# Optimization experiments

Measured on AMD Instinct MI355X. Metric: run time of the kernel, lower is better.

The kernel has to match this reference:

```python
import jax, jax.numpy as jnp
import numpy as np

N = 10000      # nodes
E = 320000     # edges (before self loops)
IN = 256
HID = 64
H = 8
OUT = 64
NEG_SLOPE = 0.2


def setup_inputs() -> dict:
    key = jax.random.key(0)
    ks = jax.random.split(key, 12)
    def glorot(k, shape):
        fan = sum(shape) if len(shape) == 2 else int(np.prod(shape))
        return jax.random.normal(k, shape, jnp.float32) * np.sqrt(2.0 / fan)
    x = jax.random.normal(ks[0], (N, IN), jnp.float32)
    edge_index = jax.random.randint(ks[1], (2, E), 0, N, jnp.int32)
    # positive weights so log2 is finite
    edge_weight = jax.random.uniform(ks[2], (E,), jnp.float32, 0.1, 1.0)
    return {
        'x': x, 'edge_index': edge_index, 'edge_weight': edge_weight,
        'W1': glorot(ks[3], (IN, H * HID)),
        'as1': glorot(ks[4], (H, HID)), 'ad1': glorot(ks[5], (H, HID)),
        'b1': jnp.zeros((H * HID,), jnp.float32),
        'W2': glorot(ks[6], (H * HID, H * OUT)),
        'as2': glorot(ks[7], (H, OUT)), 'ad2': glorot(ks[8], (H, OUT)),
        'b2': jnp.zeros((H * OUT,), jnp.float32),
    }


def _gat_conv(x, src, dst, log2_ew, W, att_src, att_dst, bias, heads, ch):
    n = x.shape[0]
    h = (x @ W).reshape(n, heads, ch)                      # [N,H,C]
    al_src = jnp.einsum('nhc,hc->nh', h, att_src)          # [N,H]
    al_dst = jnp.einsum('nhc,hc->nh', h, att_dst)
    alpha = al_src[src] + al_dst[dst]                      # [E,H]
    alpha = jax.nn.leaky_relu(alpha, NEG_SLOPE)
    alpha = alpha + log2_ew[:, None]
    # segment softmax over destination nodes (self loops ensure nonempty segments)
    amax = jax.ops.segment_max(alpha, dst, num_segments=n)
    ex = jnp.exp(alpha - amax[dst])
    denom = jax.ops.segment_sum(ex, dst, num_segments=n)
    alpha = ex / denom[dst]                                # [E,H]
    msg = h[src] * alpha[:, :, None]                       # [E,H,C]
    out = jax.ops.segment_sum(msg, dst, num_segments=n)    # [N,H,C]
    return out.reshape(n, heads * ch) + bias


def reference(x, edge_index, edge_weight, W1, as1, ad1, b1, W2, as2, ad2, b2):
    n = x.shape[0]
    # add self loops with fill_value = 1.0 (log2(1) = 0)
    loops = jnp.arange(n, dtype=edge_index.dtype)
    src = jnp.concatenate([edge_index[0], loops])
    dst = jnp.concatenate([edge_index[1], loops])
    ew = jnp.concatenate([edge_weight, jnp.ones((n,), edge_weight.dtype)])
    log2_ew = jnp.log2(ew)
    h = _gat_conv(x, src, dst, log2_ew, W1, as1, ad1, b1, H, HID)
    h = jax.nn.relu(h)  # dropout skipped (eval mode)
    out = _gat_conv(h, src, dst, log2_ew, W2, as2, ad2, b2, H, OUT)
    return out
```

## Files before the change

### kernel.cpp

```cpp
#include <hip/hip_runtime.h>
#include <hip/hip_bf16.h>

#define NN 10000
#define EE 320000
#define ETOT (EE + NN)
#define CIN 256
#define HC 512
#define NHEAD 8
#define NEG 0.2f

#define SX (NN * CIN)
#define SATT (6 * 512)

using bf16x8 = __attribute__((ext_vector_type(8))) short;
using f32x4 = __attribute__((ext_vector_type(4))) float;
typedef unsigned short u16;
typedef unsigned int u32;

__device__ __forceinline__ u16 f2bf(float f) {
  __hip_bfloat16 b = __float2bfloat16(f);
  return *(u16*)&b;
}
__device__ __forceinline__ float bflo(u32 p) { return __uint_as_float(p << 16); }
__device__ __forceinline__ float bfhi(u32 p) { return __uint_as_float(p & 0xFFFF0000u); }

#define PB_X ((SX + 255) / 256)
#define PB_ATT ((SATT + 255) / 256)
#define PB_CNT ((ETOT + 255) / 256)
#define PB_WT 96
#define PB_TOT (PB_X + PB_ATT + PB_CNT + PB_WT)

__global__ __launch_bounds__(256) void prep_k(
    const void* __restrict__ x, const void* __restrict__ w1,
    const void* __restrict__ w2,
    const void* a0, const void* a1, const void* a2,
    const void* a3, const void* a4, const void* a5,
    const int* __restrict__ ei,
    u16* __restrict__ xb, u16* __restrict__ w1t, u16* __restrict__ w2t,
    float* __restrict__ attf, int* __restrict__ counts, int* __restrict__ flag) {
  const int b = blockIdx.x, t = threadIdx.x;
  __shared__ int sbad;
  if (t == 0) sbad = 0;
  __syncthreads();
  {
    const u16* xu = (const u16*)x;
    unsigned e0 = (xu[2 * t] >> 7) & 0xFFu;
    unsigned e1 = (xu[2 * t + 1] >> 7) & 0xFFu;
    if (e0 >= 0xC8u || e1 >= 0xC8u) sbad = 1;
  }
  __syncthreads();
  const bool bf = (sbad == 0);
  if (b == 0 && t == 0) *flag = bf ? 1 : 0;

  if (b < PB_X) {
    if (!bf) {
      int i = b * 256 + t;
      if (i < SX) xb[i] = f2bf(((const float*)x)[i]);
    }
  } else if (b < PB_X + PB_ATT) {
    int j = (b - PB_X) * 256 + t;
    if (j < SATT) {
      const void* ps[6] = {a0, a1, a2, a3, a4, a5};
      const void* p = ps[j >> 9];
      int k = j & 511;
      attf[j] = bf ? __bfloat162float(((const __hip_bfloat16*)p)[k])
                   : ((const float*)p)[k];
    }
  } else if (b < PB_X + PB_ATT + PB_CNT) {
    int e = (b - PB_X - PB_ATT) * 256 + t;
    if (e < ETOT) {
      int d = (e < EE) ? ei[EE + e] : (e - EE);
      atomicAdd(&counts[d], 1);
    }
  } else {
    __shared__ u16 tile[64][72];
    int wb = b - (PB_X + PB_ATT + PB_CNT);
    const void* src;
    u16* dst;
    int K, tk, tn;
    if (wb < 32) { src = w1; dst = w1t; K = CIN; tk = (wb >> 3) * 64; tn = (wb & 7) * 64; }
    else { wb -= 32; src = w2; dst = w2t; K = HC; tk = (wb >> 3) * 64; tn = (wb & 7) * 64; }
    const int r = t >> 2, cb = (t & 3) * 16;
    if (bf) {
      const u16* s = (const u16*)src + (size_t)(tk + r) * HC + tn + cb;
      *(int4*)&tile[r][cb] = ((const int4*)s)[0];
      *(int4*)&tile[r][cb + 8] = ((const int4*)s)[1];
    } else {
      const float* s = (const float*)src + (size_t)(tk + r) * HC + tn + cb;
#pragma unroll
      for (int j = 0; j < 16; j++) tile[r][cb + j] = f2bf(s[j]);
    }
    __syncthreads();
    union { u16 o[16]; int4 v[2]; } u;
#pragma unroll
    for (int j = 0; j < 16; j++) u.o[j] = tile[cb + j][r];
    int4* dp = (int4*)(dst + (size_t)(tn + r) * K + tk + cb);
    dp[0] = u.v[0];
    dp[1] = u.v[1];
  }
}

__global__ __launch_bounds__(1024) void scan_k(const int* __restrict__ counts,
                                               int* __restrict__ rowptr,
                                               int* __restrict__ wcur) {
  __shared__ int buf[1024];
  const int t = threadIdx.x;
  int loc[10];
  int s = 0;
#pragma unroll
  for (int j = 0; j < 10; j++) {
    int i = t * 10 + j;
    s += (i < NN) ? counts[i] : 0;
    loc[j] = s;
  }
  buf[t] = s;
  __syncthreads();
  for (int off = 1; off < 1024; off <<= 1) {
    int v = (t >= off) ? buf[t - off] : 0;
    __syncthreads();
    buf[t] += v;
    __syncthreads();
  }
  int base = (t > 0) ? buf[t - 1] : 0;
  int prev = 0;
#pragma unroll
  for (int j = 0; j < 10; j++) {
    int i = t * 10 + j;
    if (i < NN) {
      rowptr[i + 1] = base + loc[j];
      wcur[i] = base + prev;
    }
    prev = loc[j];
  }
  if (t == 0) rowptr[0] = 0;
}

__global__ void fill_k(const int* __restrict__ ei, const void* __restrict__ ew,
                       const int* __restrict__ flag, int* __restrict__ wcur,
                       int* __restrict__ esrc, float* __restrict__ elw) {
  int e = blockIdx.x * blockDim.x + threadIdx.x;
  if (e >= ETOT) return;
  int s, d;
  float lw;
  if (e < EE) {
    s = ei[e];
    d = ei[EE + e];
    float w = (*flag) ? __bfloat162float(((const __hip_bfloat16*)ew)[e])
                      : ((const float*)ew)[e];
    lw = log2f(w);
  } else {
    s = d = e - EE;
    lw = 0.f;
  }
  int pos = atomicAdd(&wcur[d], 1);
  esrc[pos] = s;
  elw[pos] = lw;
}

#define BM 64
#define BN 128
#define BK 64
#define LSTR 72

__global__ __launch_bounds__(256) void gemm_mfma(const u16* __restrict__ A,
                                                 const void* __restrict__ Axalt,
                                                 const int* __restrict__ flagp,
                                                 const u16* __restrict__ Wt,
                                                 const float* __restrict__ as_w,
                                                 const float* __restrict__ ad_w,
                                                 u16* __restrict__ hb,
                                                 float* __restrict__ alsrc,
                                                 float* __restrict__ aldst,
                                                 int M, int K) {
  __shared__ u16 As[BM * LSTR];
  __shared__ u16 Bs[BN * LSTR];
  __shared__ float sps[2][2][BM], spd[2][2][BM];
  const u16* Asel = (flagp && *flagp) ? (const u16*)Axalt : A;
  const int bx = blockIdx.x;
  const int bm = blockIdx.y * BM, bn = bx * BN;
  const int t = threadIdx.x, wv = t >> 6, lane = t & 63;
  const int l15 = lane & 15, quad = lane >> 4;
  f32x4 acc[4][2] = {};
  for (int k0 = 0; k0 < K; k0 += BK) {
    {
      int row = t >> 2, kq = (t & 3) * 16;
      int gr = bm + row;
      int4 v0 = make_int4(0, 0, 0, 0), v1 = v0;
      if (gr < M) {
        const int4* gp = (const int4*)(Asel + (size_t)gr * K + k0 + kq);
        v0 = gp[0];
        v1 = gp[1];
      }
      int4* lp = (int4*)(As + row * LSTR + kq);
      lp[0] = v0;
      lp[1] = v1;
    }
    {
      int row = t >> 1, kq = (t & 1) * 32;
      const int4* gp = (const int4*)(Wt + (size_t)(bn + row) * K + k0 + kq);
      int4* lp = (int4*)(Bs + row * LSTR + kq);
      lp[0] = gp[0];
      lp[1] = gp[1];
      lp[2] = gp[2];
      lp[3] = gp[3];
    }
    __syncthreads();
#pragma unroll
    for (int kk = 0; kk < 2; kk++) {
      bf16x8 bfr[2];
#pragma unroll
      for (int ct = 0; ct < 2; ct++)
        bfr[ct] = *(const bf16x8*)(Bs + (wv * 32 + ct * 16 + l15) * LSTR + kk * 32 + quad * 8);
#pragma unroll
      for (int rt = 0; rt < 4; rt++) {
        bf16x8 af = *(const bf16x8*)(As + (rt * 16 + l15) * LSTR + kk * 32 + quad * 8);
#pragma unroll
        for (int ct = 0; ct < 2; ct++)
          acc[rt][ct] = __builtin_amdgcn_mfma_f32_16x16x32_bf16(af, bfr[ct],
                                                                acc[rt][ct], 0, 0, 0);
      }
    }
    __syncthreads();
  }
  const int head = bx * 2 + (wv >> 1);
  float asw[2], adw[2];
#pragma unroll
  for (int ct = 0; ct < 2; ct++) {
    int c = head * 64 + (wv & 1) * 32 + ct * 16 + l15;
    asw[ct] = as_w[c];
    adw[ct] = ad_w[c];
  }
#pragma unroll
  for (int rt = 0; rt < 4; rt++) {
#pragma unroll
    for (int r = 0; r < 4; r++) {
      int rib = rt * 16 + quad * 4 + r;
      int row = bm + rib;
      float ps = 0.f, pd = 0.f;
#pragma unroll
      for (int ct = 0; ct < 2; ct++) {
        float v = acc[rt][ct][r];
        ps += v * asw[ct];
        pd += v * adw[ct];
        if (row < M)
          hb[(size_t)row * HC + bn + wv * 32 + ct * 16 + l15] = f2bf(v);
      }
#pragma unroll
      for (int d = 1; d < 16; d <<= 1) {
        ps += __shfl_xor(ps, d);
        pd += __shfl_xor(pd, d);
      }
      if (l15 == 0) {
        sps[wv >> 1][wv & 1][rib] = ps;
        spd[wv >> 1][wv & 1][rib] = pd;
      }
    }
  }
  __syncthreads();
  if (t < 2 * BM) {
    int rib = t & 63, hs = t >> 6;
    int row = bm + rib;
    if (row < M) {
      alsrc[row * NHEAD + bx * 2 + hs] = sps[hs][0][rib] + sps[hs][1][rib];
      aldst[row * NHEAD + bx * 2 + hs] = spd[hs][0][rib] + spd[hs][1][rib];
    }
  }
}

#define ACC8(P, W)                                                             \
  {                                                                            \
    const u32 q0 = (u32)(P).x, q1 = (u32)(P).y, q2 = (u32)(P).z, q3 = (u32)(P).w; \
    acc[0] += (W)*bflo(q0);                                                    \
    acc[1] += (W)*bfhi(q0);                                                    \
    acc[2] += (W)*bflo(q1);                                                    \
    acc[3] += (W)*bfhi(q1);                                                    \
    acc[4] += (W)*bflo(q2);                                                    \
    acc[5] += (W)*bfhi(q2);                                                    \
    acc[6] += (W)*bflo(q3);                                                    \
    acc[7] += (W)*bfhi(q3);                                                    \
  }

template <bool RELU, bool FINAL>
__global__ __launch_bounds__(256) void agg_k(const u16* __restrict__ hb,
                                             const float* __restrict__ alsrc,
                                             const float* __restrict__ aldst,
                                             const int* __restrict__ rowptr,
                                             const int* __restrict__ esrc,
                                             const float* __restrict__ elw,
                                             const float* __restrict__ bias,
                                             u32* __restrict__ outB,
                                             float* __restrict__ outF,
                                             const int* __restrict__ flag) {
  const int n = blockIdx.x, t = threadIdx.x;
  const int lane = t & 63, wv = t >> 6;
  const int h = t & 7, eo = t >> 3;
  const int hh = lane >> 3;
  __shared__ float sw[8 * 260];
  __shared__ int ss[256];
  __shared__ float sred[32];
  __shared__ float smh[8], sd[8];
  __shared__ float red4[4][HC];
  const int beg = rowptr[n];
  const int deg = rowptr[n + 1] - beg;
  const float4 dd0 = *(const float4*)(aldst + (size_t)n * NHEAD);
  const float4 dd1 = *(const float4*)(aldst + (size_t)n * NHEAD + 4);
  const int chbase = lane * 8;
  float acc[8] = {};

  if (deg <= 256) {
    if (t < deg) {
      int e = beg + t;
      int s = esrc[e];
      float lw = elw[e];
      float4 q0 = *(const float4*)(alsrc + (size_t)s * NHEAD);
      float4 q1 = *(const float4*)(alsrc + (size_t)s * NHEAD + 4);
      float a;
      a = q0.x + dd0.x; a = (a > 0.f) ? a : NEG * a; sw[0 * 260 + t] = a + lw;
      a = q0.y + dd0.y; a = (a > 0.f) ? a : NEG * a; sw[1 * 260 + t] = a + lw;
      a = q0.z + dd0.z; a = (a > 0.f) ? a : NEG * a; sw[2 * 260 + t] = a + lw;
      a = q0.w + dd0.w; a = (a > 0.f) ? a : NEG * a; sw[3 * 260 + t] = a + lw;
      a = q1.x + dd1.x; a = (a > 0.f) ? a : NEG * a; sw[4 * 260 + t] = a + lw;
      a = q1.y + dd1.y; a = (a > 0.f) ? a : NEG * a; sw[5 * 260 + t] = a + lw;
      a = q1.z + dd1.z; a = (a > 0.f) ? a : NEG * a; sw[6 * 260 + t] = a + lw;
      a = q1.w + dd1.w; a = (a > 0.f) ? a : NEG * a; sw[7 * 260 + t] = a + lw;
      ss[t] = s;
    }
    __syncthreads();
    float m = -1e30f;
#pragma unroll
    for (int c = 0; c < 8; c++) {
      int j = c * 32 + eo;
      if (j < deg) m = fmaxf(m, sw[h * 260 + j]);
    }
    m = fmaxf(m, __shfl_xor(m, 8));
    m = fmaxf(m, __shfl_xor(m, 16));
    m = fmaxf(m, __shfl_xor(m, 32));
    if (lane < 8) sred[wv * 8 + lane] = m;
    __syncthreads();
    const float mh = fmaxf(fmaxf(sred[h], sred[8 + h]), fmaxf(sred[16 + h], sred[24 + h]));
    __syncthreads();
    float sum = 0.f;
#pragma unroll
    for (int c = 0; c < 8; c++) {
      int j = c * 32 + eo;
      if (j < deg) {
        float w = expf(sw[h * 260 + j] - mh);
        sw[h * 260 + j] = w;
        sum += w;
      }
    }
    sum += __shfl_xor(sum, 8);
    sum += __shfl_xor(sum, 16);
    sum += __shfl_xor(sum, 32);
    if (lane < 8) sred[wv * 8 + lane] = sum;
    __syncthreads();
    if (t < 8) sd[t] = sred[t] + sred[8 + t] + sred[16 + t] + sred[24 + t];
    int i = wv;
    for (; i + 12 < deg; i += 16) {
      const int s0 = ss[i], s1 = ss[i + 4], s2 = ss[i + 8], s3 = ss[i + 12];
      const float w0 = sw[hh * 260 + i], w1 = sw[hh * 260 + i + 4];
      const float w2 = sw[hh * 260 + i + 8], w3 = sw[hh * 260 + i + 12];
      const int4 p0 = *(const int4*)(hb + (size_t)s0 * HC + chbase);
      const int4 p1 = *(const int4*)(hb + (size_t)s1 * HC + chbase);
      const int4 p2 = *(const int4*)(hb + (size_t)s2 * HC + chbase);
      const int4 p3 = *(const int4*)(hb + (size_t)s3 * HC + chbase);
      ACC8(p0, w0)
      ACC8(p1, w1)
      ACC8(p2, w2)
      ACC8(p3, w3)
    }
    for (; i < deg; i += 4) {
      const int s = ss[i];
      const float w = sw[hh * 260 + i];
      const int4 p = *(const int4*)(hb + (size_t)s * HC + chbase);
      ACC8(p, w)
    }
  } else {
    const float aln = aldst[(size_t)n * NHEAD + h];
    float m = -1e30f;
    for (int j = eo; j < deg; j += 32) {
      int e = beg + j;
      float a = alsrc[(size_t)esrc[e] * NHEAD + h] + aln;
      a = (a > 0.f) ? a : NEG * a;
      m = fmaxf(m, a + elw[e]);
    }
    m = fmaxf(m, __shfl_xor(m, 8));
    m = fmaxf(m, __shfl_xor(m, 16));
    m = fmaxf(m, __shfl_xor(m, 32));
    if (lane < 8) sred[wv * 8 + lane] = m;
    __syncthreads();
    const float mh = fmaxf(fmaxf(sred[h], sred[8 + h]), fmaxf(sred[16 + h], sred[24 + h]));
    if (t < 8) smh[t] = mh;
    __syncthreads();
    float sum = 0.f;
    for (int j = eo; j < deg; j += 32) {
      int e = beg + j;
      float a = alsrc[(size_t)esrc[e] * NHEAD + h] + aln;
      a = (a > 0.f) ? a : NEG * a;
      sum += expf(a + elw[e] - mh);
    }
    sum += __shfl_xor(sum, 8);
    sum += __shfl_xor(sum, 16);
    sum += __shfl_xor(sum, 32);
    if (lane < 8) sred[wv * 8 + lane] = sum;
    __syncthreads();
    if (t < 8) sd[t] = sred[t] + sred[8 + t] + sred[16 + t] + sred[24 + t];
    for (int cb = 0; cb < deg; cb += 256) {
      int j = cb + t;
      if (j < deg) {
        int e = beg + j;
        int s = esrc[e];
        float lw = elw[e];
        float4 q0 = *(const float4*)(alsrc + (size_t)s * NHEAD);
        float4 q1 = *(const float4*)(alsrc + (size_t)s * NHEAD + 4);
        float a;
        a = q0.x + dd0.x; a = (a > 0.f) ? a : NEG * a; sw[0 * 260 + t] = expf(a + lw - smh[0]);
        a = q0.y + dd0.y; a = (a > 0.f) ? a : NEG * a; sw[1 * 260 + t] = expf(a + lw - smh[1]);
        a = q0.z + dd0.z; a = (a > 0.f) ? a : NEG * a; sw[2 * 260 + t] = expf(a + lw - smh[2]);
        a = q0.w + dd0.w; a = (a > 0.f) ? a : NEG * a; sw[3 * 260 + t] = expf(a + lw - smh[3]);
        a = q1.x + dd1.x; a = (a > 0.f) ? a : NEG * a; sw[4 * 260 + t] = expf(a + lw - smh[4]);
        a = q1.y + dd1.y; a = (a > 0.f) ? a : NEG * a; sw[5 * 260 + t] = expf(a + lw - smh[5]);
        a = q1.z + dd1.z; a = (a > 0.f) ? a : NEG * a; sw[6 * 260 + t] = expf(a + lw - smh[6]);
        a = q1.w + dd1.w; a = (a > 0.f) ? a : NEG * a; sw[7 * 260 + t] = expf(a + lw - smh[7]);
        ss[t] = s;
      }
      __syncthreads();
      int cnt = min(256, deg - cb);
      for (int i = wv; i < cnt; i += 4) {
        const int s = ss[i];
        const float w = sw[hh * 260 + i];
        const int4 p = *(const int4*)(hb + (size_t)s * HC + chbase);
        ACC8(p, w)
      }
      __syncthreads();
    }
  }
#pragma unroll
  for (int j = 0; j < 8; j++) red4[wv][chbase + j] = acc[j];
  __syncthreads();
  const int c0 = 2 * t;
  float v0 = red4[0][c0] + red4[1][c0] + red4[2][c0] + red4[3][c0];
  float v1 = red4[0][c0 + 1] + red4[1][c0 + 1] + red4[2][c0 + 1] + red4[3][c0 + 1];
  const float inv = 1.f / sd[t >> 5];
  v0 = v0 * inv + bias[c0];
  v1 = v1 * inv + bias[c0 + 1];
  if (RELU) {
    v0 = fmaxf(v0, 0.f);
    v1 = fmaxf(v1, 0.f);
  }
  if (FINAL && !(*flag)) {
    outF[(size_t)n * HC + c0] = v0;
    outF[(size_t)n * HC + c0 + 1] = v1;
  } else {
    outB[(size_t)n * (HC / 2) + t] = (u32)f2bf(v0) | ((u32)f2bf(v1) << 16);
  }
}

static constexpr size_t algn(size_t x) { return (x + 255) & ~(size_t)255; }
static constexpr size_t oFlag = 0;
static constexpr size_t oXB = algn(oFlag + 256);
static constexpr size_t oW1T = algn(oXB + (size_t)SX * 2);
static constexpr size_t oW2T = algn(oW1T + (size_t)CIN * HC * 2);
static constexpr size_t oAtt = algn(oW2T + (size_t)HC * HC * 2);
static constexpr size_t oHB = algn(oAtt + (size_t)SATT * 4);
static constexpr size_t oO1B = algn(oHB + (size_t)NN * HC * 2);
static constexpr size_t oAS = algn(oO1B + (size_t)NN * HC * 2);
static constexpr size_t oAD = algn(oAS + (size_t)NN * NHEAD * 4);
static constexpr size_t oRP = algn(oAD + (size_t)NN * NHEAD * 4);
static constexpr size_t oCnt = algn(oRP + (size_t)(NN + 1) * 4);
static constexpr size_t oWcur = algn(oCnt + (size_t)NN * 4);
static constexpr size_t oESrc = algn(oWcur + (size_t)NN * 4);
static constexpr size_t oELW = algn(oESrc + (size_t)ETOT * 4);

extern "C" void kernel_launch(void* const* d_in, const int* in_sizes, int n_in,
                              void* d_out, int out_size, void* d_ws, size_t ws_size,
                              hipStream_t stream) {
  (void)in_sizes; (void)n_in; (void)out_size; (void)ws_size;
  const int* ei = (const int*)d_in[1];

  char* ws = (char*)d_ws;
  int* flag = (int*)(ws + oFlag);
  u16* xb = (u16*)(ws + oXB);
  u16* w1t = (u16*)(ws + oW1T);
  u16* w2t = (u16*)(ws + oW2T);
  float* attf = (float*)(ws + oAtt);
  float* as1f = attf, *ad1f = attf + 512, *b1f = attf + 1024;
  float* as2f = attf + 1536, *ad2f = attf + 2048, *b2f = attf + 2560;
  u16* hb = (u16*)(ws + oHB);
  u16* o1b = (u16*)(ws + oO1B);
  float* alsrc = (float*)(ws + oAS);
  float* aldst = (float*)(ws + oAD);
  int* rowptr = (int*)(ws + oRP);
  int* counts = (int*)(ws + oCnt);
  int* wcur = (int*)(ws + oWcur);
  int* esrc = (int*)(ws + oESrc);
  float* elw = (float*)(ws + oELW);

  hipMemsetAsync(counts, 0, (size_t)NN * 4, stream);
  prep_k<<<PB_TOT, 256, 0, stream>>>(d_in[0], d_in[3], d_in[7],
                                     d_in[4], d_in[5], d_in[6],
                                     d_in[8], d_in[9], d_in[10], ei,
                                     xb, w1t, w2t, attf, counts, flag);
  scan_k<<<1, 1024, 0, stream>>>(counts, rowptr, wcur);
  fill_k<<<(ETOT + 255) / 256, 256, 0, stream>>>(ei, d_in[2], flag, wcur, esrc, elw);

  gemm_mfma<<<dim3(HC / BN, (NN + BM - 1) / BM), 256, 0, stream>>>(
      xb, d_in[0], flag, w1t, as1f, ad1f, hb, alsrc, aldst, NN, CIN);
  agg_k<true, false><<<NN, 256, 0, stream>>>(hb, alsrc, aldst, rowptr, esrc, elw,
                                             b1f, (u32*)o1b, nullptr, flag);

  gemm_mfma<<<dim3(HC / BN, (NN + BM - 1) / BM), 256, 0, stream>>>(
      o1b, nullptr, nullptr, w2t, as2f, ad2f, hb, alsrc, aldst, NN, HC);
  agg_k<false, true><<<NN, 256, 0, stream>>>(hb, alsrc, aldst, rowptr, esrc, elw,
                                             b2f, (u32*)d_out, (float*)d_out, flag);
}
```

Baseline: 263.9 us.

## Aggregate one destination node per wavefront instead of per block

The aggregation kernel now maps each 64-lane wavefront to one destination node, packing four nodes per 256-thread block. It drops the block-level __syncthreads and the cross-wave shared-memory reduction, using only wave shuffles for the softmax max and sum. Each wave processes edges sequentially, with each lane covering 8 channels. Output stores are vectorized to 16 bytes. The trade-off is less memory-level parallelism per node, since edges are walked serially by one wave, and the high-degree fallback recomputes attention per edge.

```diff
diff --git a/kernel.cpp b/kernel.cpp
--- a/kernel.cpp
+++ b/kernel.cpp
@@ -291,75 +291,52 @@
                                              u32* __restrict__ outB,
                                              float* __restrict__ outF,
                                              const int* __restrict__ flag) {
-  const int n = blockIdx.x, t = threadIdx.x;
-  const int lane = t & 63, wv = t >> 6;
-  const int h = t & 7, eo = t >> 3;
+  const int t = threadIdx.x;
+  const int wv = t >> 6, lane = t & 63;
+  const int n = blockIdx.x * 4 + wv;
+  const int h = lane & 7, eo = lane >> 3;
   const int hh = lane >> 3;
-  __shared__ float sw[8 * 260];
-  __shared__ int ss[256];
-  __shared__ float sred[32];
-  __shared__ float smh[8], sd[8];
-  __shared__ float red4[4][HC];
+  const int chbase = lane * 8;
+  __shared__ float swA[4][NHEAD][132];
+  __shared__ int ssA[4][128];
+  float (*const swv)[132] = swA[wv];
+  int* const ssv = ssA[wv];
   const int beg = rowptr[n];
   const int deg = rowptr[n + 1] - beg;
-  const float4 dd0 = *(const float4*)(aldst + (size_t)n * NHEAD);
-  const float4 dd1 = *(const float4*)(aldst + (size_t)n * NHEAD + 4);
-  const int chbase = lane * 8;
+  const float aln = aldst[(size_t)n * NHEAD + h];
   float acc[8] = {};
-
-  if (deg <= 256) {
-    if (t < deg) {
-      int e = beg + t;
+  float inv;
+
+  if (deg <= 128) {
+    float m = -1e30f;
+    for (int j = eo; j < deg; j += 8) {
+      int e = beg + j;
       int s = esrc[e];
-      float lw = elw[e];
-      float4 q0 = *(const float4*)(alsrc + (size_t)s * NHEAD);
-      float4 q1 = *(const float4*)(alsrc + (size_t)s * NHEAD + 4);
-      float a;
-      a = q0.x + dd0.x; a = (a > 0.f) ? a : NEG * a; sw[0 * 260 + t] = a + lw;
-      a = q0.y + dd0.y; a = (a > 0.f) ? a : NEG * a; sw[1 * 260 + t] = a + lw;
-      a = q0.z + dd0.z; a = (a > 0.f) ? a : NEG * a; sw[2 * 260 + t] = a + lw;
-      a = q0.w + dd0.w; a = (a > 0.f) ? a : NEG * a; sw[3 * 260 + t] = a + lw;
-      a = q1.x + dd1.x; a = (a > 0.f) ? a : NEG * a; sw[4 * 260 + t] = a + lw;
-      a = q1.y + dd1.y; a = (a > 0.f) ? a : NEG * a; sw[5 * 260 + t] = a + lw;
-      a = q1.z + dd1.z; a = (a > 0.f) ? a : NEG * a; sw[6 * 260 + t] = a + lw;
-      a = q1.w + dd1.w; a = (a > 0.f) ? a : NEG * a; sw[7 * 260 + t] = a + lw;
-      ss[t] = s;
-    }
-    __syncthreads();
-    float m = -1e30f;
-#pragma unroll
-    for (int c = 0; c < 8; c++) {
-      int j = c * 32 + eo;
-      if (j < deg) m = fmaxf(m, sw[h * 260 + j]);
+      float a = alsrc[(size_t)s * NHEAD + h] + aln;
+      a = (a > 0.f) ? a : NEG * a;
+      a += elw[e];
+      swv[h][j] = a;
+      m = fmaxf(m, a);
+      if (h == 0) ssv[j] = s;
     }
     m = fmaxf(m, __shfl_xor(m, 8));
     m = fmaxf(m, __shfl_xor(m, 16));
     m = fmaxf(m, __shfl_xor(m, 32));
-    if (lane < 8) sred[wv * 8 + lane] = m;
-    __syncthreads();
-    const float mh = fmaxf(fmaxf(sred[h], sred[8 + h]), fmaxf(sred[16 + h], sred[24 + h]));
-    __syncthreads();
     float sum = 0.f;
-#pragma unroll
-    for (int c = 0; c < 8; c++) {
-      int j = c * 32 + eo;
-      if (j < deg) {
-        float w = expf(sw[h * 260 + j] - mh);
-        sw[h * 260 + j] = w;
-        sum += w;
-      }
+    for (int j = eo; j < deg; j += 8) {
+      float w = expf(swv[h][j] - m);
+      swv[h][j] = w;
+      sum += w;
     }
     sum += __shfl_xor(sum, 8);
     sum += __shfl_xor(sum, 16);
     sum += __shfl_xor(sum, 32);
-    if (lane < 8) sred[wv * 8 + lane] = sum;
-    __syncthreads();
-    if (t < 8) sd[t] = sred[t] + sred[8 + t] + sred[16 + t] + sred[24 + t];
-    int i = wv;
-    for (; i + 12 < deg; i += 16) {
-      const int s0 = ss[i], s1 = ss[i + 4], s2 = ss[i + 8], s3 = ss[i + 12];
-      const float w0 = sw[hh * 260 + i], w1 = sw[hh * 260 + i + 4];
-      const float w2 = sw[hh * 260 + i + 8], w3 = sw[hh * 260 + i + 12];
+    inv = 1.f / __shfl(sum, hh);
+    int i = 0;
+    for (; i + 3 < deg; i += 4) {
+      const int s0 = ssv[i], s1 = ssv[i + 1], s2 = ssv[i + 2], s3 = ssv[i + 3];
+      const float w0 = swv[hh][i], w1 = swv[hh][i + 1];
+      const float w2 = swv[hh][i + 2], w3 = swv[hh][i + 3];
       const int4 p0 = *(const int4*)(hb + (size_t)s0 * HC + chbase);
       const int4 p1 = *(const int4*)(hb + (size_t)s1 * HC + chbase);
       const int4 p2 = *(const int4*)(hb + (size_t)s2 * HC + chbase);
@@ -369,16 +346,15 @@
       ACC8(p2, w2)
       ACC8(p3, w3)
     }
-    for (; i < deg; i += 4) {
-      const int s = ss[i];
-      const float w = sw[hh * 260 + i];
+    for (; i < deg; i++) {
+      const int s = ssv[i];
+      const float w = swv[hh][i];
       const int4 p = *(const int4*)(hb + (size_t)s * HC + chbase);
       ACC8(p, w)
     }
   } else {
-    const float aln = aldst[(size_t)n * NHEAD + h];
     float m = -1e30f;
-    for (int j = eo; j < deg; j += 32) {
+    for (int j = eo; j < deg; j += 8) {
       int e = beg + j;
       float a = alsrc[(size_t)esrc[e] * NHEAD + h] + aln;
       a = (a > 0.f) ? a : NEG * a;
@@ -387,72 +363,51 @@
     m = fmaxf(m, __shfl_xor(m, 8));
     m = fmaxf(m, __shfl_xor(m, 16));
     m = fmaxf(m, __shfl_xor(m, 32));
-    if (lane < 8) sred[wv * 8 + lane] = m;
-    __syncthreads();
-    const float mh = fmaxf(fmaxf(sred[h], sred[8 + h]), fmaxf(sred[16 + h], sred[24 + h]));
-    if (t < 8) smh[t] = mh;
-    __syncthreads();
     float sum = 0.f;
-    for (int j = eo; j < deg; j += 32) {
+    for (int j = eo; j < deg; j += 8) {
       int e = beg + j;
       float a = alsrc[(size_t)esrc[e] * NHEAD + h] + aln;
       a = (a > 0.f) ? a : NEG * a;
-      sum += expf(a + elw[e] - mh);
+      sum += expf(a + elw[e] - m);
     }
     sum += __shfl_xor(sum, 8);
     sum += __shfl_xor(sum, 16);
     sum += __shfl_xor(sum, 32);
-    if (lane < 8) sred[wv * 8 + lane] = sum;
-    __syncthreads();
-    if (t < 8) sd[t] = sred[t] + sred[8 + t] + sred[16 + t] + sred[24 + t];
-    for (int cb = 0; cb < deg; cb += 256) {
-      int j = cb + t;
-      if (j < deg) {
-        int e = beg + j;
-        int s = esrc[e];
-        float lw = elw[e];
-        float4 q0 = *(const float4*)(alsrc + (size_t)s * NHEAD);
-        float4 q1 = *(const float4*)(alsrc + (size_t)s * NHEAD + 4);
-        float a;
-        a = q0.x + dd0.x; a = (a > 0.f) ? a : NEG * a; sw[0 * 260 + t] = expf(a + lw - smh[0]);
-        a = q0.y + dd0.y; a = (a > 0.f) ? a : NEG * a; sw[1 * 260 + t] = expf(a + lw - smh[1]);
-        a = q0.z + dd0.z; a = (a > 0.f) ? a : NEG * a; sw[2 * 260 + t] = expf(a + lw - smh[2]);
-        a = q0.w + dd0.w; a = (a > 0.f) ? a : NEG * a; sw[3 * 260 + t] = expf(a + lw - smh[3]);
-        a = q1.x + dd1.x; a = (a > 0.f) ? a : NEG * a; sw[4 * 260 + t] = expf(a + lw - smh[4]);
-        a = q1.y + dd1.y; a = (a > 0.f) ? a : NEG * a; sw[5 * 260 + t] = expf(a + lw - smh[5]);
-        a = q1.z + dd1.z; a = (a > 0.f) ? a : NEG * a; sw[6 * 260 + t] = expf(a + lw - smh[6]);
-        a = q1.w + dd1.w; a = (a > 0.f) ? a : NEG * a; sw[7 * 260 + t] = expf(a + lw - smh[7]);
-        ss[t] = s;
-      }
-      __syncthreads();
-      int cnt = min(256, deg - cb);
-      for (int i = wv; i < cnt; i += 4) {
-        const int s = ss[i];
-        const float w = sw[hh * 260 + i];
-        const int4 p = *(const int4*)(hb + (size_t)s * HC + chbase);
-        ACC8(p, w)
-      }
-      __syncthreads();
-    }
-  }
-#pragma unroll
-  for (int j = 0; j < 8; j++) red4[wv][chbase + j] = acc[j];
-  __syncthreads();
-  const int c0 = 2 * t;
-  float v0 = red4[0][c0] + red4[1][c0] + red4[2][c0] + red4[3][c0];
-  float v1 = red4[0][c0 + 1] + red4[1][c0 + 1] + red4[2][c0 + 1] + red4[3][c0 + 1];
-  const float inv = 1.f / sd[t >> 5];
-  v0 = v0 * inv + bias[c0];
-  v1 = v1 * inv + bias[c0 + 1];
+    inv = 1.f / __shfl(sum, hh);
+    const float mh = __shfl(m, hh);
+    const float alnh = __shfl(aln, hh);
+    for (int i = 0; i < deg; i++) {
+      int e = beg + i;
+      int s = esrc[e];
+      float a = alsrc[(size_t)s * NHEAD + hh] + alnh;
+      a = (a > 0.f) ? a : NEG * a;
+      float w = expf(a + elw[e] - mh);
+      const int4 p = *(const int4*)(hb + (size_t)s * HC + chbase);
+      ACC8(p, w)
+    }
+  }
+  const float4 b0 = *(const float4*)(bias + chbase);
+  const float4 b1 = *(const float4*)(bias + chbase + 4);
+  float v[8];
+  v[0] = acc[0] * inv + b0.x; v[1] = acc[1] * inv + b0.y;
+  v[2] = acc[2] * inv + b0.z; v[3] = acc[3] * inv + b0.w;
+  v[4] = acc[4] * inv + b1.x; v[5] = acc[5] * inv + b1.y;
+  v[6] = acc[6] * inv + b1.z; v[7] = acc[7] * inv + b1.w;
   if (RELU) {
-    v0 = fmaxf(v0, 0.f);
-    v1 = fmaxf(v1, 0.f);
+#pragma unroll
+    for (int k = 0; k < 8; k++) v[k] = fmaxf(v[k], 0.f);
   }
   if (FINAL && !(*flag)) {
-    outF[(size_t)n * HC + c0] = v0;
-    outF[(size_t)n * HC + c0 + 1] = v1;
+    float4* op = (float4*)(outF + (size_t)n * HC + chbase);
+    op[0] = make_float4(v[0], v[1], v[2], v[3]);
+    op[1] = make_float4(v[4], v[5], v[6], v[7]);
   } else {
-    outB[(size_t)n * (HC / 2) + t] = (u32)f2bf(v0) | ((u32)f2bf(v1) << 16);
+    int4 pk;
+    pk.x = (int)((u32)f2bf(v[0]) | ((u32)f2bf(v[1]) << 16));
+    pk.y = (int)((u32)f2bf(v[2]) | ((u32)f2bf(v[3]) << 16));
+    pk.z = (int)((u32)f2bf(v[4]) | ((u32)f2bf(v[5]) << 16));
+    pk.w = (int)((u32)f2bf(v[6]) | ((u32)f2bf(v[7]) << 16));
+    *(int4*)(outB + (size_t)n * (HC / 2) + lane * 4) = pk;
   }
 }
 
@@ -506,11 +461,11 @@
 
   gemm_mfma<<<dim3(HC / BN, (NN + BM - 1) / BM), 256, 0, stream>>>(
       xb, d_in[0], flag, w1t, as1f, ad1f, hb, alsrc, aldst, NN, CIN);
-  agg_k<true, false><<<NN, 256, 0, stream>>>(hb, alsrc, aldst, rowptr, esrc, elw,
-                                             b1f, (u32*)o1b, nullptr, flag);
+  agg_k<true, false><<<NN / 4, 256, 0, stream>>>(hb, alsrc, aldst, rowptr, esrc, elw,
+                                                 b1f, (u32*)o1b, nullptr, flag);
 
   gemm_mfma<<<dim3(HC / BN, (NN + BM - 1) / BM), 256, 0, stream>>>(
       o1b, nullptr, nullptr, w2t, as2f, ad2f, hb, alsrc, aldst, NN, HC);
-  agg_k<false, true><<<NN, 256, 0, stream>>>(hb, alsrc, aldst, rowptr, esrc, elw,
-                                             b2f, (u32*)d_out, (float*)d_out, flag);
-}
+  agg_k<false, true><<<NN / 4, 256, 0, stream>>>(hb, alsrc, aldst, rowptr, esrc, elw,
+                                                 b2f, (u32*)d_out, (float*)d_out, flag);
+}
```

After: 259.4 us. Within noise of the previous version (-1.7%).
